# Kernel tuning notes

Hardware: AMD Instinct MI355X
Metric: run time of the kernel (lower is better)

Reference implementation:

```python
import jax, jax.numpy as jnp
import numpy as np

B, L, D_MODEL, D_MEM = 4, 8192, 512, 512
SSM_DIM = D_MODEL + D_MEM


def setup_inputs() -> dict:
    key = jax.random.key(0)
    ks = jax.random.split(key, 4)
    s = 0.02
    return {
        "x": jax.random.normal(ks[0], (B, L, D_MODEL), dtype=jnp.float32),
        "W_av": jax.random.normal(ks[1], (4 * D_MEM, D_MODEL), dtype=jnp.float32) * s,
        "b_av": jnp.zeros((4 * D_MEM,), dtype=jnp.float32),
        "W_go": jax.random.normal(ks[2], (D_MODEL, SSM_DIM), dtype=jnp.float32) * s,
        "b_go": jnp.zeros((D_MODEL,), dtype=jnp.float32),
        "W_out": jax.random.normal(ks[3], (2 * D_MODEL, D_MODEL), dtype=jnp.float32) * s,
        "b_out": jnp.zeros((2 * D_MODEL,), dtype=jnp.float32),
    }


def reference(x, W_av, b_av, W_go, b_go, W_out, b_out):
    d = D_MEM
    b = x.shape[0]
    # alpha_v = Linear(d_model -> 4*d_memory) on x[:, :-1]
    av = jnp.einsum("bld,kd->blk", x[:, :-1], W_av) + b_av
    # NRU memory update: alpha+*v+ - alpha-*v-  (all nonlins default to identity)
    ms_inp = av[..., :d] * av[..., d:2 * d] - av[..., 2 * d:3 * d] * av[..., 3 * d:4 * d]
    # associative cumsum scan along length, prefixed with zero initial memory
    ms = jnp.cumsum(ms_inp, axis=1)
    m_init = jnp.zeros((b, 1, d), dtype=x.dtype)
    ms = jnp.concatenate([m_init, ms], axis=1)  # [b, L, d_memory]
    ssm_inp = jnp.concatenate([x, ms], axis=2)  # [b, L, ssm_dim]
    # SSM sublayer (external registry module) stubbed as identity
    ssm_out = ssm_inp
    y = jnp.einsum("blk,dk->bld", ssm_out, W_go) + b_go  # gated_out
    y = jax.nn.gelu(y, approximate=False)  # activation='gelu' (torch exact erf)
    z = jnp.einsum("bld,kd->blk", y, W_out) + b_out  # [b, L, 2*d_model]
    y = z[..., :D_MODEL] * jax.nn.sigmoid(z[..., D_MODEL:])
    return y
```

## Files before the change

### kernel.cpp

```cpp
#include <hip/hip_runtime.h>
#include <hip/hip_bf16.h>
#include <math.h>

#define B_SZ 4
#define L_SZ 8192
#define DM 512
#define DMEM 512
#define M1 (B_SZ * (L_SZ - 1))
#define M2 (B_SZ * L_SZ)

typedef _Float16 h16;
typedef __attribute__((ext_vector_type(2))) _Float16 f16x2;
typedef __attribute__((ext_vector_type(8))) _Float16 f16x8;
typedef __attribute__((ext_vector_type(4))) float f32x4;

#define MFMA16(a, b, c) __builtin_amdgcn_mfma_f32_16x16x32_f16((a), (b), (c), 0, 0, 0)
#define WAVES_EU(mn, mx) __attribute__((amdgpu_waves_per_eu(mn, mx)))

__device__ __forceinline__ void gl16(const void* g, void* l) {
    __builtin_amdgcn_global_load_lds(
        (const __attribute__((address_space(1))) void*)g,
        (__attribute__((address_space(3))) void*)l, 16, 0, 0);
}

__device__ __forceinline__ f16x8 lds_frag(const h16* base, int row, int col, int key) {
    return *(const f16x8*)((const char*)base + row * 128 + ((col * 2) ^ (key << 4)));
}

__device__ __forceinline__ void xcd_remap(int& bx, int& by) {
    int gx = gridDim.x, gy = gridDim.y;
    int nwg = gx * gy;
    int lin = blockIdx.y * gx + blockIdx.x;
    int chunk = nwg >> 3;
    int l = (lin & 7) * chunk + (lin >> 3);
    by = l % gy;
    bx = l / gy;
}

__global__ __launch_bounds__(256) void prep_all(
    const float* __restrict__ x, const float* __restrict__ Wgo,
    const float* __restrict__ Wav, const float* __restrict__ Wout,
    h16* __restrict__ xh, h16* __restrict__ Wgoh,
    h16* __restrict__ Wavh, h16* __restrict__ Wouth)
{
    int i = blockIdx.x * 256 + threadIdx.x;
    const float* s;
    h16* d;
    if (i < 2097152) {
        int m = i >> 6, bb = i & 63;
        s = x + (size_t)m * 512 + bb * 8;
        d = xh + (size_t)m * 512 + (bb ^ (m & 7)) * 8;
    } else {
        int j = i - 2097152;
        if (j < 65536) {
            int r = j >> 7, bb = j & 127;
            s = Wgo + (size_t)r * 1024 + bb * 8;
            d = Wgoh + (size_t)r * 1024 + (bb ^ (r & 7)) * 8;
        } else if (j < 196608) {
            int k = j - 65536;
            int P = k >> 6, bb = k & 63;
            int by = P >> 7, lo = P & 127;
            int half = lo >> 6, g = (lo >> 4) & 3, nl = lo & 15;
            int orig = g * 512 + by * 32 + half * 16 + nl;
            s = Wav + (size_t)orig * 512 + bb * 8;
            d = Wavh + (size_t)P * 512 + (bb ^ (P & 7)) * 8;
        } else {
            int k = j - 196608;
            int P = k >> 6, bb = k & 63;
            int by = P >> 7, lo = P & 127;
            int chunk = lo >> 5, g = (lo >> 4) & 1, nl = lo & 15;
            int orig = g * 512 + by * 64 + chunk * 16 + nl;
            s = Wout + (size_t)orig * 512 + bb * 8;
            d = Wouth + (size_t)P * 512 + (bb ^ (P & 7)) * 8;
        }
    }
    const float4* sv = (const float4*)s;
    float4 v0 = sv[0], v1 = sv[1];
    float vv[8] = {v0.x, v0.y, v0.z, v0.w, v1.x, v1.y, v1.z, v1.w};
    f16x8 hh;
    #pragma unroll
    for (int j = 0; j < 8; ++j) hh[j] = (h16)vv[j];
    *(f16x8*)d = hh;
}

#define PIPE_WAIT(N) do { \
    asm volatile("s_waitcnt vmcnt(" #N ")" ::: "memory"); \
    __builtin_amdgcn_s_barrier(); \
    asm volatile("" ::: "memory"); \
} while (0)
#define PIPE_POST() do { \
    __builtin_amdgcn_s_barrier(); \
    asm volatile("" ::: "memory"); \
} while (0)

__global__ __launch_bounds__(256) WAVES_EU(3, 3) void gemm_av_mfma(
    const h16* __restrict__ xh, const h16* __restrict__ Wh,
    const float* __restrict__ bav, h16* __restrict__ ms_inp)
{
    __shared__ __align__(16) h16 As[128 * 64];
    __shared__ __align__(16) h16 Bh[128 * 64];

    int bx, by; xcd_remap(bx, by);
    const int tid = threadIdx.x, lane = tid & 63, w = tid >> 6;
    const int wm = (w & 1) * 64, wn = (w >> 1) * 64;
    const int bm = bx * 128;
    const int ln = lane & 15, ko = (lane >> 4) * 8;
    const int kb = ln & 7;
    char* lA = (char*)As; char* lH = (char*)Bh;
    const int wb = w * 1024;

    const char *aP[4], *hP[4];
    {
        const int r8 = lane >> 3, c16 = (lane & 7) * 16;
        #pragma unroll
        for (int i = 0; i < 4; ++i) {
            int row = i * 32 + w * 8 + r8;
            int mg = bm + row; if (mg > M1 - 1) mg = M1 - 1;
            size_t xr = (size_t)mg + (unsigned)mg / (L_SZ - 1);
            aP[i] = (const char*)xh + xr * (DM * 2) + c16;
            size_t br = (size_t)(by * 128 + row) * (DM * 2) + c16;
            hP[i] = (const char*)Wh + br;
        }
    }
    int ka[4];
    #pragma unroll
    for (int fm = 0; fm < 4; ++fm) {
        int m = bm + wm + fm * 16 + ln;
        int mg = m > M1 - 1 ? M1 - 1 : m;
        ka[fm] = (int)((mg + (unsigned)mg / (L_SZ - 1)) & 7);
    }

    f32x4 acc[4][4];
    #pragma unroll
    for (int i = 0; i < 4; ++i)
        #pragma unroll
        for (int j = 0; j < 4; ++j) acc[i][j] = (f32x4){0.f, 0.f, 0.f, 0.f};

#define STAGE_AV(koff) do { \
    gl16(aP[0] + (koff), lA + 0 * 4096 + wb); gl16(hP[0] + (koff), lH + 0 * 4096 + wb); \
    gl16(aP[1] + (koff), lA + 1 * 4096 + wb); gl16(hP[1] + (koff), lH + 1 * 4096 + wb); \
    gl16(aP[2] + (koff), lA + 2 * 4096 + wb); gl16(hP[2] + (koff), lH + 2 * 4096 + wb); \
    gl16(aP[3] + (koff), lA + 3 * 4096 + wb); gl16(hP[3] + (koff), lH + 3 * 4096 + wb); \
} while (0)

    STAGE_AV(0);
    for (int kt = 0; kt < 8; ++kt) {
        asm volatile("s_waitcnt vmcnt(0)" ::: "memory");
        __syncthreads();
        #pragma unroll
        for (int s = 0; s < 2; ++s) {
            const int c = s * 32 + ko;
            f16x8 a[4];
            #pragma unroll
            for (int fm = 0; fm < 4; ++fm)
                a[fm] = lds_frag(As, wm + fm * 16 + ln, c, ka[fm]);
            #pragma unroll
            for (int fn = 0; fn < 4; ++fn) {
                f16x8 vh = lds_frag(Bh, wn + fn * 16 + ln, c, kb);
                #pragma unroll
                for (int fm = 0; fm < 4; ++fm)
                    acc[fm][fn] = MFMA16(a[fm], vh, acc[fm][fn]);
            }
        }
        __syncthreads();
        if (kt < 7) STAGE_AV((kt + 1) * 128);
    }
#undef STAGE_AV

    const int lm = (lane >> 4) * 4;
    const int nn = by * 32 + (wn >> 6) * 16 + ln;
    const float b0 = bav[nn], b1 = bav[nn + 512], b2 = bav[nn + 1024], b3 = bav[nn + 1536];
    #pragma unroll
    for (int fm = 0; fm < 4; ++fm) {
        #pragma unroll
        for (int i = 0; i < 4; ++i) {
            int m = bm + wm + fm * 16 + lm + i;
            if (m < M1) {
                float a0 = acc[fm][0][i] + b0;
                float a1 = acc[fm][1][i] + b1;
                float a2 = acc[fm][2][i] + b2;
                float a3 = acc[fm][3][i] + b3;
                ms_inp[(size_t)m * DMEM + nn] = (h16)(a0 * a1 - a2 * a3);
            }
        }
    }
}

__global__ __launch_bounds__(256) void scan_pass1(
    const h16* __restrict__ ms_inp, float* __restrict__ csum)
{
    int b = blockIdx.y;
    int c = blockIdx.x * 4 + (threadIdx.x >> 6);
    int t = threadIdx.x & 63;
    int l0 = c * 32;
    int len = min(32, (L_SZ - 1) - l0);
    const h16* p = ms_inp + ((size_t)b * (L_SZ - 1) + l0) * DMEM + t * 8;
    float s[8] = {0.f, 0.f, 0.f, 0.f, 0.f, 0.f, 0.f, 0.f};
    for (int i = 0; i < len; ++i) {
        f16x8 v = *(const f16x8*)(p + (size_t)i * DMEM);
        #pragma unroll
        for (int j = 0; j < 8; ++j) s[j] += (float)v[j];
    }
    float* q = csum + ((size_t)b * 256 + c) * DMEM + t * 8;
    *(float4*)q       = make_float4(s[0], s[1], s[2], s[3]);
    *(float4*)(q + 4) = make_float4(s[4], s[5], s[6], s[7]);
}

__global__ __launch_bounds__(256) void scan_pass2(float* __restrict__ csum)
{
    __shared__ float wsum[4];
    int b = blockIdx.x >> 9, d = blockIdx.x & 511;
    int t = threadIdx.x, lane = t & 63, wv = t >> 6;
    float* p = csum + (size_t)b * 256 * DMEM + d;
    float v = p[(size_t)t * DMEM];
    #pragma unroll
    for (int off = 1; off < 64; off <<= 1) {
        float u = __shfl_up(v, off, 64);
        if (lane >= off) v += u;
    }
    if (lane == 63) wsum[wv] = v;
    __syncthreads();
    float add = 0.f;
    #pragma unroll
    for (int i = 0; i < 4; ++i) if (i < wv) add += wsum[i];
    v += add;
    float ex = __shfl_up(v, 1, 64);
    if (lane == 0) ex = add;
    p[(size_t)t * DMEM] = ex;
}

__global__ __launch_bounds__(256) void scan_pass3(
    const h16* __restrict__ ms_inp, const float* __restrict__ csum,
    h16* __restrict__ msh)
{
    int b = blockIdx.y;
    int c = blockIdx.x * 4 + (threadIdx.x >> 6);
    int t = threadIdx.x & 63;
    int l0 = c * 32;
    int len = min(32, (L_SZ - 1) - l0);
    const float* q = csum + ((size_t)b * 256 + c) * DMEM + t * 8;
    float run[8];
    #pragma unroll
    for (int j = 0; j < 8; ++j) run[j] = q[j];
    const h16* p = ms_inp + ((size_t)b * (L_SZ - 1) + l0) * DMEM + t * 8;
    if (c == 0) {
        f16x8 z = {};
        *(f16x8*)(msh + (size_t)b * L_SZ * DMEM + t * 8) = z;
    }
    for (int i = 0; i < len; ++i) {
        f16x8 v = *(const f16x8*)(p + (size_t)i * DMEM);
        f16x8 o;
        #pragma unroll
        for (int j = 0; j < 8; ++j) { run[j] += (float)v[j]; o[j] = (h16)run[j]; }
        int m = b * L_SZ + l0 + 1 + i;
        int db = t ^ (m & 7);
        *(f16x8*)(msh + (size_t)m * DMEM + db * 8) = o;
    }
}

__global__ __launch_bounds__(256) WAVES_EU(2, 2) void gemm_go_mfma(
    const h16* __restrict__ xh, const h16* __restrict__ msh,
    const h16* __restrict__ Wh,
    const float* __restrict__ bgo, h16* __restrict__ yh)
{
    __shared__ __align__(16) h16 As[2][128 * 64];
    __shared__ __align__(16) h16 Bh[2][128 * 64];

    int bx, by; xcd_remap(bx, by);
    const int tid = threadIdx.x, lane = tid & 63, w = tid >> 6;
    const int wm = (w & 1) * 64, wn = (w >> 1) * 64;
    const int bm = bx * 128, bn = by * 128;
    const int ln = lane & 15, ko = (lane >> 4) * 8;
    const int kk = ln & 7;
    const int wb = w * 1024;

    const char *xP[4], *mP[4], *hP[4];
    {
        const int r8 = lane >> 3, c16 = (lane & 7) * 16;
        #pragma unroll
        for (int i = 0; i < 4; ++i) {
            int row = i * 32 + w * 8 + r8;
            size_t ar = (size_t)(bm + row) * (DM * 2) + c16;
            xP[i] = (const char*)xh + ar;
            mP[i] = (const char*)msh + ar;
            size_t br = (size_t)(bn + row) * (2 * DM * 2) + c16;
            hP[i] = (const char*)Wh + br;
        }
    }

    f32x4 acc[4][4];
    #pragma unroll
    for (int i = 0; i < 4; ++i)
        #pragma unroll
        for (int j = 0; j < 4; ++j) acc[i][j] = (f32x4){0.f, 0.f, 0.f, 0.f};

#define STAGE_GO(tt, sel) do { \
    char* dA = (char*)As[sel]; char* dB = (char*)Bh[sel]; \
    const int bo = (tt) * 128; \
    if ((tt) < 8) { \
        const int ao = (tt) * 128; \
        gl16(xP[0] + ao, dA + 0 * 4096 + wb); gl16(hP[0] + bo, dB + 0 * 4096 + wb); \
        gl16(xP[1] + ao, dA + 1 * 4096 + wb); gl16(hP[1] + bo, dB + 1 * 4096 + wb); \
        gl16(xP[2] + ao, dA + 2 * 4096 + wb); gl16(hP[2] + bo, dB + 2 * 4096 + wb); \
        gl16(xP[3] + ao, dA + 3 * 4096 + wb); gl16(hP[3] + bo, dB + 3 * 4096 + wb); \
    } else { \
        const int ao = ((tt) - 8) * 128; \
        gl16(mP[0] + ao, dA + 0 * 4096 + wb); gl16(hP[0] + bo, dB + 0 * 4096 + wb); \
        gl16(mP[1] + ao, dA + 1 * 4096 + wb); gl16(hP[1] + bo, dB + 1 * 4096 + wb); \
        gl16(mP[2] + ao, dA + 2 * 4096 + wb); gl16(hP[2] + bo, dB + 2 * 4096 + wb); \
        gl16(mP[3] + ao, dA + 3 * 4096 + wb); gl16(hP[3] + bo, dB + 3 * 4096 + wb); \
    } \
} while (0)

    STAGE_GO(0, 0);
    STAGE_GO(1, 1);
    for (int kt = 0; kt < 16; ++kt) {
        if (kt < 15) PIPE_WAIT(8); else PIPE_WAIT(0);
        const h16* A = As[kt & 1];
        const h16* B = Bh[kt & 1];
        #pragma unroll
        for (int s = 0; s < 2; ++s) {
            const int c = s * 32 + ko;
            f16x8 a[4];
            #pragma unroll
            for (int fm = 0; fm < 4; ++fm)
                a[fm] = lds_frag(A, wm + fm * 16 + ln, c, kk);
            #pragma unroll
            for (int fn = 0; fn < 4; ++fn) {
                f16x8 vh = lds_frag(B, wn + fn * 16 + ln, c, kk);
                #pragma unroll
                for (int fm = 0; fm < 4; ++fm)
                    acc[fm][fn] = MFMA16(a[fm], vh, acc[fm][fn]);
            }
        }
        PIPE_POST();
        if (kt + 2 < 16) STAGE_GO(kt + 2, kt & 1);
    }
#undef STAGE_GO

    const int lm = (lane >> 4) * 4;
    #pragma unroll
    for (int fm = 0; fm < 4; ++fm) {
        #pragma unroll
        for (int fn = 0; fn < 4; ++fn) {
            int n = bn + wn + fn * 16 + ln;
            float bias = bgo[n];
            #pragma unroll
            for (int i = 0; i < 4; ++i) {
                int m = bm + wm + fm * 16 + lm + i;
                float t = acc[fm][fn][i] + bias;
                float g = 0.5f * t * (1.0f + erff(t * 0.70710678118654752f));
                int nsw = (((n >> 3) ^ (m & 7)) << 3) | (n & 7);
                yh[(size_t)m * DM + nsw] = (h16)g;
            }
        }
    }
}

__global__ __launch_bounds__(256) WAVES_EU(2, 2) void gemm_out_mfma(
    const h16* __restrict__ yh, const h16* __restrict__ Wh,
    const float* __restrict__ bout, float* __restrict__ out)
{
    __shared__ __align__(16) h16 As[2][128 * 64];
    __shared__ __align__(16) h16 Bh[2][128 * 64];

    int bx, by; xcd_remap(bx, by);
    const int tid = threadIdx.x, lane = tid & 63, w = tid >> 6;
    const int wm = (w & 1) * 64, wn = (w >> 1) * 64;
    const int bm = bx * 128;
    const int ln = lane & 15, ko = (lane >> 4) * 8;
    const int kk = ln & 7;
    const int wb = w * 1024;

    const char *aP[4], *hP[4];
    {
        const int r8 = lane >> 3, c16 = (lane & 7) * 16;
        #pragma unroll
        for (int i = 0; i < 4; ++i) {
            int row = i * 32 + w * 8 + r8;
            aP[i] = (const char*)yh + (size_t)(bm + row) * (DM * 2) + c16;
            size_t br = (size_t)(by * 128 + row) * (DM * 2) + c16;
            hP[i] = (const char*)Wh + br;
        }
    }

    f32x4 acc[4][4];
    #pragma unroll
    for (int i = 0; i < 4; ++i)
        #pragma unroll
        for (int j = 0; j < 4; ++j) acc[i][j] = (f32x4){0.f, 0.f, 0.f, 0.f};

#define STAGE_OUT(koff, sel) do { \
    char* dA = (char*)As[sel]; char* dB = (char*)Bh[sel]; \
    gl16(aP[0] + (koff), dA + 0 * 4096 + wb); gl16(hP[0] + (koff), dB + 0 * 4096 + wb); \
    gl16(aP[1] + (koff), dA + 1 * 4096 + wb); gl16(hP[1] + (koff), dB + 1 * 4096 + wb); \
    gl16(aP[2] + (koff), dA + 2 * 4096 + wb); gl16(hP[2] + (koff), dB + 2 * 4096 + wb); \
    gl16(aP[3] + (koff), dA + 3 * 4096 + wb); gl16(hP[3] + (koff), dB + 3 * 4096 + wb); \
} while (0)

    STAGE_OUT(0, 0);
    STAGE_OUT(128, 1);
    for (int kt = 0; kt < 8; ++kt) {
        if (kt < 7) PIPE_WAIT(8); else PIPE_WAIT(0);
        const h16* A = As[kt & 1];
        const h16* B = Bh[kt & 1];
        #pragma unroll
        for (int s = 0; s < 2; ++s) {
            const int c = s * 32 + ko;
            f16x8 a[4];
            #pragma unroll
            for (int fm = 0; fm < 4; ++fm)
                a[fm] = lds_frag(A, wm + fm * 16 + ln, c, kk);
            #pragma unroll
            for (int fn = 0; fn < 4; ++fn) {
                f16x8 vh = lds_frag(B, wn + fn * 16 + ln, c, kk);
                #pragma unroll
                for (int fm = 0; fm < 4; ++fm)
                    acc[fm][fn] = MFMA16(a[fm], vh, acc[fm][fn]);
            }
        }
        PIPE_POST();
        if (kt + 2 < 8) STAGE_OUT((kt + 2) * 128, kt & 1);
    }
#undef STAGE_OUT

    const int lm = (lane >> 4) * 4;
    #pragma unroll
    for (int fm = 0; fm < 4; ++fm) {
        #pragma unroll
        for (int cp = 0; cp < 2; ++cp) {
            int ncol = by * 64 + ((wn >> 5) + cp) * 16 + ln;
            float bz0 = bout[ncol], bz1 = bout[ncol + 512];
            #pragma unroll
            for (int i = 0; i < 4; ++i) {
                int m = bm + wm + fm * 16 + lm + i;
                float z0 = acc[fm][cp * 2 + 0][i] + bz0;
                float z1 = acc[fm][cp * 2 + 1][i] + bz1;
                out[(size_t)m * DM + ncol] = z0 * (1.0f / (1.0f + expf(-z1)));
            }
        }
    }
}

extern "C" void kernel_launch(void* const* d_in, const int* in_sizes, int n_in,
                              void* d_out, int out_size, void* d_ws, size_t ws_size,
                              hipStream_t stream)
{
    const float* x    = (const float*)d_in[0];
    const float* Wav  = (const float*)d_in[1];
    const float* bav  = (const float*)d_in[2];
    const float* Wgo  = (const float*)d_in[3];
    const float* bgo  = (const float*)d_in[4];
    const float* Wout = (const float*)d_in[5];
    const float* bout = (const float*)d_in[6];
    float* out = (float*)d_out;

    char* ws = (char*)d_ws;
    const size_t MB = 1 << 20;
    h16*   ms_inp = (h16*)ws;
    h16*   yh     = (h16*)(ws + 32 * MB);
    h16*   xh     = (h16*)(ws + 64 * MB);
    h16*   msh    = (h16*)(ws + 96 * MB);
    h16*   Wavh   = (h16*)(ws + 129 * MB);
    h16*   Wgoh   = (h16*)(ws + 131 * MB);
    h16*   Wouth  = (h16*)(ws + 132 * MB);
    float* csum   = (float*)(ws + 133 * MB);

    prep_all<<<9216, 256, 0, stream>>>(x, Wgo, Wav, Wout, xh, Wgoh, Wavh, Wouth);
    gemm_av_mfma<<<dim3(256, 16), 256, 0, stream>>>(xh, Wavh, bav, ms_inp);
    scan_pass1<<<dim3(64, B_SZ), 256, 0, stream>>>(ms_inp, csum);
    scan_pass2<<<2048, 256, 0, stream>>>(csum);
    scan_pass3<<<dim3(64, B_SZ), 256, 0, stream>>>(ms_inp, csum, msh);
    gemm_go_mfma<<<dim3(256, 4), 256, 0, stream>>>(xh, msh, Wgoh, bgo, yh);
    gemm_out_mfma<<<dim3(256, 8), 256, 0, stream>>>(yh, Wouth, bout, out);
}
```

Baseline: 233.4 us.

## Enlarge av GEMM tile to 256x256 with double-buffered LDS prefetch

Restructures the first GEMM to use 512-thread blocks computing 256x256 output tiles, with the weight permutation in prep changed to match. LDS is double buffered so the next K slice loads while the current one is computed, and s_setprio wraps the MFMA bursts. Each wave now holds an 8x4 accumulator tile and keeps B fragments in registers, which raises data reuse per LDS read. The cost is higher register and LDS pressure, lower occupancy (2 waves/EU), and fewer blocks (1024), which may leave the machine less evenly loaded.

Measured after the change: 232.9 us. About the same (-0.2%).

```diff
diff --git a/kernel.cpp b/kernel.cpp
--- a/kernel.cpp
+++ b/kernel.cpp
@@ -59,9 +59,9 @@
         } else if (j < 196608) {
             int k = j - 65536;
             int P = k >> 6, bb = k & 63;
-            int by = P >> 7, lo = P & 127;
-            int half = lo >> 6, g = (lo >> 4) & 3, nl = lo & 15;
-            int orig = g * 512 + by * 32 + half * 16 + nl;
+            int by = P >> 8, lo = P & 255;
+            int c = lo >> 6, g = (lo >> 4) & 3, nl = lo & 15;
+            int orig = g * 512 + by * 64 + c * 16 + nl;
             s = Wav + (size_t)orig * 512 + bb * 8;
             d = Wavh + (size_t)P * 512 + (bb ^ (P & 7)) * 8;
         } else {
@@ -93,88 +93,113 @@
     asm volatile("" ::: "memory"); \
 } while (0)
 
-__global__ __launch_bounds__(256) WAVES_EU(3, 3) void gemm_av_mfma(
+__global__ __launch_bounds__(512) WAVES_EU(2, 2) void gemm_av_mfma(
     const h16* __restrict__ xh, const h16* __restrict__ Wh,
     const float* __restrict__ bav, h16* __restrict__ ms_inp)
 {
-    __shared__ __align__(16) h16 As[128 * 64];
-    __shared__ __align__(16) h16 Bh[128 * 64];
+    __shared__ __align__(16) h16 As[2][2][128 * 64];
+    __shared__ __align__(16) h16 Bs[2][2][128 * 64];
 
     int bx, by; xcd_remap(bx, by);
     const int tid = threadIdx.x, lane = tid & 63, w = tid >> 6;
-    const int wm = (w & 1) * 64, wn = (w >> 1) * 64;
-    const int bm = bx * 128;
+    const int wr = w >> 2;
+    const int wc = w & 3;
+    const int bm = bx * 256;
     const int ln = lane & 15, ko = (lane >> 4) * 8;
     const int kb = ln & 7;
-    char* lA = (char*)As; char* lH = (char*)Bh;
-    const int wb = w * 1024;
-
-    const char *aP[4], *hP[4];
+    const int bhalf = wc >> 1;
+    const int brow0 = (wc & 1) * 64;
+
+    const char *aS[2][2], *bS[2][2];
     {
-        const int r8 = lane >> 3, c16 = (lane & 7) * 16;
-        #pragma unroll
-        for (int i = 0; i < 4; ++i) {
-            int row = i * 32 + w * 8 + r8;
-            int mg = bm + row; if (mg > M1 - 1) mg = M1 - 1;
-            size_t xr = (size_t)mg + (unsigned)mg / (L_SZ - 1);
-            aP[i] = (const char*)xh + xr * (DM * 2) + c16;
-            size_t br = (size_t)(by * 128 + row) * (DM * 2) + c16;
-            hP[i] = (const char*)Wh + br;
-        }
-    }
-    int ka[4];
-    #pragma unroll
-    for (int fm = 0; fm < 4; ++fm) {
-        int m = bm + wm + fm * 16 + ln;
+        const int r = tid >> 3, cb = tid & 7;
+        #pragma unroll
+        for (int h = 0; h < 2; ++h)
+            #pragma unroll
+            for (int i = 0; i < 2; ++i) {
+                int row = h * 128 + i * 64 + r;
+                int mg = bm + row; if (mg > M1 - 1) mg = M1 - 1;
+                size_t xr = (size_t)mg + (unsigned)mg / (L_SZ - 1);
+                aS[h][i] = (const char*)xh + xr * 1024 + cb * 16;
+                int P = by * 256 + row;
+                bS[h][i] = (const char*)Wh + (size_t)P * 1024 + cb * 16;
+            }
+    }
+    int ka[8];
+    #pragma unroll
+    for (int fm = 0; fm < 8; ++fm) {
+        int m = bm + wr * 128 + fm * 16 + ln;
         int mg = m > M1 - 1 ? M1 - 1 : m;
         ka[fm] = (int)((mg + (unsigned)mg / (L_SZ - 1)) & 7);
     }
 
-    f32x4 acc[4][4];
-    #pragma unroll
-    for (int i = 0; i < 4; ++i)
+    f32x4 acc[8][4];
+    #pragma unroll
+    for (int i = 0; i < 8; ++i)
         #pragma unroll
         for (int j = 0; j < 4; ++j) acc[i][j] = (f32x4){0.f, 0.f, 0.f, 0.f};
 
-#define STAGE_AV(koff) do { \
-    gl16(aP[0] + (koff), lA + 0 * 4096 + wb); gl16(hP[0] + (koff), lH + 0 * 4096 + wb); \
-    gl16(aP[1] + (koff), lA + 1 * 4096 + wb); gl16(hP[1] + (koff), lH + 1 * 4096 + wb); \
-    gl16(aP[2] + (koff), lA + 2 * 4096 + wb); gl16(hP[2] + (koff), lH + 2 * 4096 + wb); \
-    gl16(aP[3] + (koff), lA + 3 * 4096 + wb); gl16(hP[3] + (koff), lH + 3 * 4096 + wb); \
+#define STAGE_T(dd, koff) do { \
+    char* lA = (char*)As + (dd) * 32768 + w * 1024; \
+    char* lB = (char*)Bs + (dd) * 32768 + w * 1024; \
+    gl16(aS[0][0] + (koff), lA);                 gl16(bS[0][0] + (koff), lB); \
+    gl16(aS[0][1] + (koff), lA + 8192);          gl16(bS[0][1] + (koff), lB + 8192); \
+    gl16(aS[1][0] + (koff), lA + 16384);         gl16(bS[1][0] + (koff), lB + 16384); \
+    gl16(aS[1][1] + (koff), lA + 24576);         gl16(bS[1][1] + (koff), lB + 24576); \
 } while (0)
 
-    STAGE_AV(0);
-    for (int kt = 0; kt < 8; ++kt) {
-        asm volatile("s_waitcnt vmcnt(0)" ::: "memory");
-        __syncthreads();
-        #pragma unroll
-        for (int s = 0; s < 2; ++s) {
-            const int c = s * 32 + ko;
-            f16x8 a[4];
-            #pragma unroll
-            for (int fm = 0; fm < 4; ++fm)
-                a[fm] = lds_frag(As, wm + fm * 16 + ln, c, ka[fm]);
-            #pragma unroll
-            for (int fn = 0; fn < 4; ++fn) {
-                f16x8 vh = lds_frag(Bh, wn + fn * 16 + ln, c, kb);
+    STAGE_T(0, 0);
+    for (int t = 0; t < 8; ++t) {
+        const int d = t & 1;
+        __builtin_amdgcn_s_barrier();
+        asm volatile("" ::: "memory");
+        if (t < 7) {
+            STAGE_T(d ^ 1, (t + 1) * 128);
+            asm volatile("s_waitcnt vmcnt(8)" ::: "memory");
+        } else {
+            asm volatile("s_waitcnt vmcnt(0)" ::: "memory");
+        }
+        __builtin_amdgcn_s_barrier();
+        asm volatile("" ::: "memory");
+
+        const h16* A = &As[d][wr][0];
+        const h16* B = &Bs[d][bhalf][0];
+        f16x8 bf[4][2];
+        #pragma unroll
+        for (int fn = 0; fn < 4; ++fn)
+            #pragma unroll
+            for (int ks = 0; ks < 2; ++ks)
+                bf[fn][ks] = lds_frag(B, brow0 + fn * 16 + ln, ks * 32 + ko, kb);
+        #pragma unroll
+        for (int p = 0; p < 4; ++p) {
+            f16x8 a[2][2];
+            #pragma unroll
+            for (int j = 0; j < 2; ++j)
                 #pragma unroll
-                for (int fm = 0; fm < 4; ++fm)
-                    acc[fm][fn] = MFMA16(a[fm], vh, acc[fm][fn]);
-            }
-        }
-        __syncthreads();
-        if (kt < 7) STAGE_AV((kt + 1) * 128);
-    }
-#undef STAGE_AV
+                for (int ks = 0; ks < 2; ++ks)
+                    a[j][ks] = lds_frag(A, (2 * p + j) * 16 + ln, ks * 32 + ko, ka[2 * p + j]);
+            __builtin_amdgcn_s_setprio(1);
+            #pragma unroll
+            for (int j = 0; j < 2; ++j)
+                #pragma unroll
+                for (int fn = 0; fn < 4; ++fn)
+                    #pragma unroll
+                    for (int ks = 0; ks < 2; ++ks)
+                        acc[2 * p + j][fn] = MFMA16(a[j][ks], bf[fn][ks], acc[2 * p + j][fn]);
+            __builtin_amdgcn_s_setprio(0);
+            __builtin_amdgcn_sched_barrier(0);
+        }
+    }
+#undef STAGE_T
 
     const int lm = (lane >> 4) * 4;
-    const int nn = by * 32 + (wn >> 6) * 16 + ln;
+    const int nn = by * 64 + wc * 16 + ln;
     const float b0 = bav[nn], b1 = bav[nn + 512], b2 = bav[nn + 1024], b3 = bav[nn + 1536];
     #pragma unroll
-    for (int fm = 0; fm < 4; ++fm) {
+    for (int fm = 0; fm < 8; ++fm) {
         #pragma unroll
         for (int i = 0; i < 4; ++i) {
-            int m = bm + wm + fm * 16 + lm + i;
+            int m = bm + wr * 128 + fm * 16 + lm + i;
             if (m < M1) {
                 float a0 = acc[fm][0][i] + b0;
                 float a1 = acc[fm][1][i] + b1;
@@ -467,7 +492,7 @@
     float* csum   = (float*)(ws + 133 * MB);
 
     prep_all<<<9216, 256, 0, stream>>>(x, Wgo, Wav, Wout, xh, Wgoh, Wavh, Wouth);
-    gemm_av_mfma<<<dim3(256, 16), 256, 0, stream>>>(xh, Wavh, bav, ms_inp);
+    gemm_av_mfma<<<dim3(128, 8), 512, 0, stream>>>(xh, Wavh, bav, ms_inp);
     scan_pass1<<<dim3(64, B_SZ), 256, 0, stream>>>(ms_inp, csum);
     scan_pass2<<<2048, 256, 0, stream>>>(csum);
     scan_pass3<<<dim3(64, B_SZ), 256, 0, stream>>>(ms_inp, csum, msh);
```
